# Kernel optimization log

Measured on AMD Instinct MI355X. Metric: run time of the kernel, lower is better.

## Reference

```python
import jax, jax.numpy as jnp
import numpy as np

DIM = 1024
HEADS = 16
HEAD_DIM = DIM // HEADS
B, N, S = 4, 4096, 512


def setup_inputs() -> dict:
    key = jax.random.key(0)
    ks = jax.random.split(key, 9)
    scale = DIM ** -0.5
    return {
        "x": jax.random.normal(ks[0], (B, N, DIM), dtype=jnp.float32),
        "context": jax.random.normal(ks[1], (B, S, DIM), dtype=jnp.float32),
        "context_mask": jax.random.uniform(ks[2], (B, S)) < 0.2,  # True = padding
        "q_w": jax.random.normal(ks[3], (DIM, DIM), dtype=jnp.float32) * scale,
        "q_b": jnp.zeros((DIM,), dtype=jnp.float32),
        "kv_w": jax.random.normal(ks[4], (DIM, 2 * DIM), dtype=jnp.float32) * scale,
        "kv_b": jnp.zeros((2 * DIM,), dtype=jnp.float32),
        "proj_w": jax.random.normal(ks[5], (DIM, DIM), dtype=jnp.float32) * scale,
        "proj_b": jnp.zeros((DIM,), dtype=jnp.float32),
    }


def reference(x, context, context_mask, q_w, q_b, kv_w, kv_b, proj_w, proj_b):
    b, n, c = x.shape
    s = context.shape[1]
    h, d = HEADS, HEAD_DIM
    scale = d ** -0.5

    # projections
    q = (x @ q_w + q_b).reshape(b, n, h, d)            # [B,N,H,D]
    kv = (context @ kv_w + kv_b).reshape(b, s, 2, h, d)
    k = kv[:, :, 0]                                     # [B,S,H,D]
    v = kv[:, :, 1]

    # scores [B,H,N,S]
    attn = jnp.einsum("bnhd,bshd->bhns", q, k) * scale
    attn = jnp.where(context_mask[:, None, None, :], -jnp.inf, attn)
    attn = jax.nn.softmax(attn, axis=-1)

    out = jnp.einsum("bhns,bshd->bnhd", attn, v).reshape(b, n, c)
    return out @ proj_w + proj_b
```

## Files before the change

kernel.cpp:

```cpp
#include <hip/hip_runtime.h>
#include <hip/hip_bf16.h>

typedef __attribute__((ext_vector_type(8))) short bf16x8;
typedef __attribute__((ext_vector_type(4))) float f32x4;
typedef unsigned short u16;

#define DIMC 1024
#define NHEAD 16
#define HDIM 64
#define NB 4
#define NQ 4096
#define NS 512

#define LOG2E 1.44269504f

#if __has_builtin(__builtin_amdgcn_exp2f)
#define EXP2F(x) __builtin_amdgcn_exp2f(x)
#else
#define EXP2F(x) __expf(0.69314718f * (x))
#endif

#if __has_builtin(__builtin_amdgcn_rcpf)
#define RCPF(x) __builtin_amdgcn_rcpf(x)
#else
#define RCPF(x) (1.0f / (x))
#endif

__device__ __forceinline__ u16 f2bf(float f) {
  __hip_bfloat16 h = __float2bfloat16(f);
  return *reinterpret_cast<u16*>(&h);
}

__device__ __forceinline__ unsigned pack_bf2(float a, float b) {
  __hip_bfloat162 h2 = __float22bfloat162_rn(make_float2(a, b));
  return *reinterpret_cast<unsigned*>(&h2);
}

__device__ __forceinline__ void gload_lds16(const void* g, void* s) {
  __builtin_amdgcn_global_load_lds(
      (const __attribute__((address_space(1))) void*)g,
      (__attribute__((address_space(3))) void*)s, 16, 0, 0);
}


__device__ __forceinline__ void cvt_body(const float* __restrict__ in,
                                         u16* __restrict__ out, int base, int nblk,
                                         int n4) {
  const int stride = nblk * 256;
  for (int i = base * 256 + threadIdx.x; i < n4; i += stride) {
    float4 v = *(const float4*)(in + (size_t)i * 4);
    ushort4 o;
    o.x = f2bf(v.x); o.y = f2bf(v.y); o.z = f2bf(v.z); o.w = f2bf(v.w);
    *(ushort4*)(out + (size_t)i * 4) = o;
  }
}

__global__ void prep_kernel(const float* __restrict__ x, const float* __restrict__ ctx,
                            const int* __restrict__ cmask,
                            const float* __restrict__ q_w, const float* __restrict__ kv_w,
                            const float* __restrict__ proj_w,
                            u16* __restrict__ x_bf, u16* __restrict__ ctx_bf,
                            u16* __restrict__ qwT, u16* __restrict__ kvwT,
                            u16* __restrict__ pwT, float* __restrict__ maskf) {
  __shared__ float t[32][33];
  const int bid = blockIdx.x;
  if (bid < 2048) {
    cvt_body(x, x_bf, bid, 2048, 16777216 / 4);
    return;
  }
  if (bid < 2560) {
    cvt_body(ctx, ctx_bf, bid - 2048, 512, 2097152 / 4);
    return;
  }
  if (bid >= 6656) {
    const int i = (bid - 6656) * 256 + threadIdx.x;
    if (i < NB * NS) maskf[i] = cmask[i] ? -1e30f : 0.0f;
    return;
  }
  const float* W;
  u16* WT;
  int K, N, local;
  if (bid < 3584) {
    W = q_w; WT = qwT; K = 1024; N = 1024; local = bid - 2560;
  } else if (bid < 5632) {
    W = kv_w; WT = kvwT; K = 1024; N = 2048; local = bid - 3584;
  } else {
    W = proj_w; WT = pwT; K = 1024; N = 1024; local = bid - 5632;
  }
  const int nbx = N >> 5;
  const int bx = (local % nbx) * 32;
  const int by = (local / nbx) * 32;
  const int tx = threadIdx.x & 31, ty = threadIdx.x >> 5;
#pragma unroll
  for (int i = 0; i < 32; i += 8)
    t[ty + i][tx] = W[(size_t)(by + ty + i) * N + bx + tx];
  __syncthreads();
#pragma unroll
  for (int i = 0; i < 32; i += 8)
    WT[(size_t)(bx + ty + i) * K + by + tx] = f2bf(t[tx][ty + i]);
}


__launch_bounds__(256)
__global__ void gemm_kv(const u16* __restrict__ A, const u16* __restrict__ BT,
                        const float* __restrict__ bias, u16* __restrict__ Kout,
                        u16* __restrict__ VTout, int M, int N, int K) {
  __shared__ __align__(16) u16 As[128 * 32];
  __shared__ __align__(16) u16 Bs[128 * 32];
  const int tid = threadIdx.x;
  const int w = tid >> 6, l = tid & 63;
  const int wr = w >> 1, wc = w & 1;
  const int fr = l & 15, fhi = l >> 4;

  const int nwg = gridDim.x * gridDim.y;
  const int o = blockIdx.y * gridDim.x + blockIdx.x;
  const int tIdx = (o & 7) * (nwg >> 3) + (o >> 3);
  const int m0 = (tIdx / gridDim.x) * 128;
  const int n0 = (tIdx % gridDim.x) * 128;

  const f32x4 fz = {0.f, 0.f, 0.f, 0.f};
  f32x4 acc[4][4];
#pragma unroll
  for (int mt = 0; mt < 4; mt++)
#pragma unroll
    for (int nt = 0; nt < 4; nt++) acc[mt][nt] = fz;

  const int f0 = w * 2048 + l * 16;
  const int f1 = f0 + 1024;
  const int ar0 = f0 >> 6, ac0 = (f0 & 63) >> 1;
  const int ar1 = f1 >> 6, ac1 = (f1 & 63) >> 1;
  const u16* Ag0 = A + (size_t)(m0 + ar0) * K + ac0;
  const u16* Ag1 = A + (size_t)(m0 + ar1) * K + ac1;
  const u16* Bg0 = BT + (size_t)(n0 + ar0) * K + ac0;
  const u16* Bg1 = BT + (size_t)(n0 + ar1) * K + ac1;

  for (int k0 = 0; k0 < K; k0 += 32) {
    gload_lds16(Ag0 + k0, &As[w * 1024]);
    gload_lds16(Ag1 + k0, &As[w * 1024 + 512]);
    gload_lds16(Bg0 + k0, &Bs[w * 1024]);
    gload_lds16(Bg1 + k0, &Bs[w * 1024 + 512]);
    __syncthreads();

    bf16x8 a[4], b[4];
#pragma unroll
    for (int t = 0; t < 4; t++) {
      a[t] = *(const bf16x8*)&As[(wr * 64 + t * 16 + fr) * 32 + fhi * 8];
      b[t] = *(const bf16x8*)&Bs[(wc * 64 + t * 16 + fr) * 32 + fhi * 8];
    }
#pragma unroll
    for (int mt = 0; mt < 4; mt++)
#pragma unroll
      for (int nt = 0; nt < 4; nt++)
        acc[mt][nt] = __builtin_amdgcn_mfma_f32_16x16x32_bf16(a[mt], b[nt], acc[mt][nt], 0, 0, 0);
    __syncthreads();
  }

#pragma unroll
  for (int mt = 0; mt < 4; mt++) {
#pragma unroll
    for (int nt = 0; nt < 4; nt++) {
      const int col = n0 + wc * 64 + nt * 16 + fr;
      const float bv = bias[col];
#pragma unroll
      for (int r = 0; r < 4; r++) {
        const int row = m0 + wr * 64 + mt * 16 + fhi * 4 + r;
        const float v = acc[mt][nt][r] + bv;
        const int b = row >> 9, s = row & 511;
        if (col < 1024) {
          const int h = col >> 6, d = col & 63;
          Kout[(((size_t)(b * 16 + h)) * 512 + s) * 64 + d] = f2bf(v);
        } else {
          const int c2 = col - 1024;
          const int h = c2 >> 6, d = c2 & 63;
          VTout[(((size_t)(b * 16 + h)) * 64 + d) * 512 + s] = f2bf(v);
        }
      }
    }
  }
}


template<int MODE>
__launch_bounds__(512, 1)
__global__ void gemm256(const u16* __restrict__ A, const u16* __restrict__ BT,
                        const float* __restrict__ bias, void* __restrict__ C0,
                        int M, int N, int K) {
  __shared__ __align__(16) u16 As[2][16384];
  __shared__ __align__(16) u16 Bs[2][16384];
  const int tid = threadIdx.x;
  const int w = tid >> 6, l = tid & 63;
  const int wm = w >> 2, wn = w & 3;
  const int fr = l & 15, fhi = l >> 4;

  const int nblk = gridDim.x;
  const int nN = N >> 8;
  const int o = blockIdx.x;
  const int tIdx = (o & 7) * (nblk >> 3) + (o >> 3);
  const int m0 = (tIdx / nN) << 8;
  const int n0 = (tIdx % nN) << 8;

  const int rowoff = tid >> 3;
  const int gchunk = (tid & 7) ^ (rowoff & 7);
  const u16* Abase = A + (size_t)(m0 + rowoff) * K + gchunk * 8;
  const u16* Bbase = BT + (size_t)(n0 + rowoff) * K + gchunk * 8;
  const int ldsoff = w * 512;

  const f32x4 fz = {0.f, 0.f, 0.f, 0.f};
  f32x4 acc[2][4][4];
#pragma unroll
  for (int mh = 0; mh < 2; mh++)
#pragma unroll
    for (int m = 0; m < 4; m++)
#pragma unroll
      for (int n = 0; n < 4; n++) acc[mh][m][n] = fz;

  const int KT = K >> 6;

#pragma unroll
  for (int p = 0; p < 4; ++p) {
    gload_lds16(Abase + (size_t)(p * 64) * K, &As[0][p * 4096 + ldsoff]);
    gload_lds16(Bbase + (size_t)(p * 64) * K, &Bs[0][p * 4096 + ldsoff]);
  }
  asm volatile("s_waitcnt vmcnt(0)" ::: "memory");
  __builtin_amdgcn_s_barrier();

  int nb = 0;
  for (int kt = 0; kt < KT; ++kt) {
    const int knext = (kt + 1) << 6;
    const bool more = (kt + 1) < KT;
#pragma unroll
    for (int p = 0; p < 4; ++p) {
      const int mh = p >> 1, kk = p & 1;
      const int ch = ((kk << 2) | fhi) ^ (fr & 7);
      bf16x8 af[4], bfr[4];
#pragma unroll
      for (int m = 0; m < 4; ++m) {
        const int row = wm * 128 + mh * 64 + m * 16 + fr;
        af[m] = *(const bf16x8*)((const char*)&As[nb][0] + row * 128 + ch * 16);
      }
#pragma unroll
      for (int n = 0; n < 4; ++n) {
        const int row = wn * 64 + n * 16 + fr;
        bfr[n] = *(const bf16x8*)((const char*)&Bs[nb][0] + row * 128 + ch * 16);
      }
      if (more) {
        gload_lds16(Abase + (size_t)(p * 64) * K + knext, &As[nb ^ 1][p * 4096 + ldsoff]);
        gload_lds16(Bbase + (size_t)(p * 64) * K + knext, &Bs[nb ^ 1][p * 4096 + ldsoff]);
      }
      __builtin_amdgcn_s_barrier();
      asm volatile("s_waitcnt lgkmcnt(0)" ::: "memory");
      __builtin_amdgcn_s_setprio(1);
#pragma unroll
      for (int m = 0; m < 4; ++m)
#pragma unroll
        for (int n = 0; n < 4; ++n)
          acc[mh][m][n] = __builtin_amdgcn_mfma_f32_16x16x32_bf16(af[m], bfr[n], acc[mh][m][n], 0, 0, 0);
      __builtin_amdgcn_s_setprio(0);
      __builtin_amdgcn_s_barrier();
    }
    asm volatile("s_waitcnt vmcnt(0)" ::: "memory");
    __builtin_amdgcn_s_barrier();
    nb ^= 1;
  }

#pragma unroll
  for (int mh = 0; mh < 2; ++mh)
#pragma unroll
    for (int m = 0; m < 4; ++m)
#pragma unroll
      for (int n = 0; n < 4; ++n) {
        const int col = n0 + wn * 64 + n * 16 + fr;
        const float bv = bias[col];
#pragma unroll
        for (int r = 0; r < 4; ++r) {
          const int row = m0 + wm * 128 + mh * 64 + m * 16 + fhi * 4 + r;
          const float v = acc[mh][m][n][r] + bv;
          if (MODE == 0)
            ((u16*)C0)[(size_t)row * N + col] = f2bf(v * 0.125f);
          else
            ((float*)C0)[(size_t)row * N + col] = v;
        }
      }
}

__launch_bounds__(512, 2)
__global__ void attn_kernel(const u16* __restrict__ Q, const u16* __restrict__ Kb,
                            const u16* __restrict__ VT, const float* __restrict__ maskf,
                            u16* __restrict__ O) {
  __shared__ __align__(16) u16 Ks[512 * 64];
  __shared__ __align__(16) u16 Vs[64 * 512];
  __shared__ __align__(16) u16 Ps[8][2048];
  const int tid = threadIdx.x, w = tid >> 6, l = tid & 63;
  const int fr = l & 15, fhi = l >> 4;

  const int rid = blockIdx.x;
  const int orig = ((rid & 7) << 5) + (rid >> 3);
  const int bh = orig >> 2, qc = orig & 3;
  const int b = bh >> 4, h = bh & 15;

  const u16* Kg = Kb + (size_t)bh * NS * HDIM;
  const u16* Vg = VT + (size_t)bh * HDIM * NS;
  const float* mrow = maskf + b * NS;

#pragma unroll
  for (int it = 0; it < 8; ++it) {
    const int slot = it * 512 + tid;
    const int r = slot >> 3, c3 = slot & 7;
    const int gc = c3 ^ (r & 7);
    gload_lds16(Kg + (size_t)r * HDIM + gc * 8, &Ks[slot * 8]);
  }
#pragma unroll
  for (int it = 0; it < 8; ++it) {
    const int slot = it * 512 + tid;
    const int r = slot >> 6, c6 = slot & 63;
    const int gc = c6 ^ (r & 7);
    gload_lds16(Vg + (size_t)r * NS + gc * 8, &Vs[slot * 8]);
  }
  asm volatile("s_waitcnt vmcnt(0)" ::: "memory");
  __syncthreads();

  u16* Pw = Ps[w];
  const f32x4 fz = {0.f, 0.f, 0.f, 0.f};

  bf16x8 onesf;
#pragma unroll
  for (int i = 0; i < 8; ++i) onesf[i] = (short)0x3F80;

#pragma unroll 1
  for (int qt2 = 0; qt2 < 2; ++qt2) {
    const int rowbase_a = b * NQ + qc * 1024 + w * 128 + qt2 * 64;
    const int rowbase_b = rowbase_a + 32;

    bf16x8 qfa[2][2], qfb[2][2];
#pragma unroll
    for (int mt = 0; mt < 2; mt++)
#pragma unroll
      for (int kk = 0; kk < 2; kk++) {
        qfa[mt][kk] = *(const bf16x8*)&Q[(size_t)(rowbase_a + mt * 16 + fr) * DIMC +
                                         h * 64 + kk * 32 + fhi * 8];
        qfb[mt][kk] = *(const bf16x8*)&Q[(size_t)(rowbase_b + mt * 16 + fr) * DIMC +
                                         h * 64 + kk * 32 + fhi * 8];
      }

    f32x4 lacc_a[2], lacc_b[2];
    f32x4 oa[2][4], ob[2][4];
#pragma unroll
    for (int mt = 0; mt < 2; mt++) {
      lacc_a[mt] = fz; lacc_b[mt] = fz;
#pragma unroll
      for (int dn = 0; dn < 4; dn++) { oa[mt][dn] = fz; ob[mt][dn] = fz; }
    }

#pragma unroll
    for (int t = 0; t < 8; ++t) {
      const int sc = t * 64;

      bf16x8 kf[2][4];
#pragma unroll
      for (int kk = 0; kk < 2; kk++)
#pragma unroll
        for (int sn = 0; sn < 4; sn++) {
          const int row = sc + sn * 16 + fr;
          const int byte = row * 128 + ((((kk << 2) | fhi) ^ (fr & 7)) << 4);
          kf[kk][sn] = *(const bf16x8*)((const char*)&Ks[0] + byte);
        }

      f32x4 sa[2][4];
#pragma unroll
      for (int mt = 0; mt < 2; mt++)
#pragma unroll
        for (int sn = 0; sn < 4; sn++) sa[mt][sn] = fz;
      __builtin_amdgcn_s_setprio(1);
#pragma unroll
      for (int kk = 0; kk < 2; kk++)
#pragma unroll
        for (int sn = 0; sn < 4; sn++)
#pragma unroll
          for (int mt = 0; mt < 2; mt++)
            sa[mt][sn] = __builtin_amdgcn_mfma_f32_16x16x32_bf16(kf[kk][sn], qfa[mt][kk], sa[mt][sn], 0, 0, 0);
      __builtin_amdgcn_s_setprio(0);

      float4 mv4[4];
#pragma unroll
      for (int sn = 0; sn < 4; sn++)
        mv4[sn] = *(const float4*)&mrow[sc + sn * 16 + fhi * 4];

#pragma unroll
      for (int mt = 0; mt < 2; mt++) {
        const int qrow = mt * 16 + fr;
#pragma unroll
        for (int sn = 0; sn < 4; sn++) {
          const float e0 = EXP2F(fmaf(sa[mt][sn][0], LOG2E, ((const float*)&mv4[sn])[0]));
          const float e1 = EXP2F(fmaf(sa[mt][sn][1], LOG2E, ((const float*)&mv4[sn])[1]));
          const float e2 = EXP2F(fmaf(sa[mt][sn][2], LOG2E, ((const float*)&mv4[sn])[2]));
          const float e3 = EXP2F(fmaf(sa[mt][sn][3], LOG2E, ((const float*)&mv4[sn])[3]));
          int byte = qrow * 128 + sn * 32 + fhi * 8;
          byte ^= (qrow & 7) << 4;
          uint2 pk;
          pk.x = pack_bf2(e0, e1);
          pk.y = pack_bf2(e2, e3);
          *(uint2*)((char*)Pw + byte) = pk;
        }
      }
      asm volatile("s_waitcnt lgkmcnt(0)" ::: "memory");

      bf16x8 vv[2][4];
#pragma unroll
      for (int kk = 0; kk < 2; kk++)
#pragma unroll
        for (int dn = 0; dn < 4; dn++) {
          const int row = dn * 16 + fr;
          const int byte = row * 1024 +
              (((sc >> 3) + ((((kk << 2) | fhi) ^ (fr & 7)))) << 4);
          vv[kk][dn] = *(const bf16x8*)((const char*)&Vs[0] + byte);
        }

      __builtin_amdgcn_s_setprio(1);
#pragma unroll
      for (int kk = 0; kk < 2; kk++)
#pragma unroll
        for (int mt = 0; mt < 2; mt++) {
          int byte = (mt * 16 + fr) * 128 + kk * 64 + fhi * 16;
          byte ^= (fr & 7) << 4;
          const bf16x8 pa = *(const bf16x8*)((char*)Pw + byte);
#pragma unroll
          for (int dn = 0; dn < 4; dn++)
            oa[mt][dn] = __builtin_amdgcn_mfma_f32_16x16x32_bf16(pa, vv[kk][dn], oa[mt][dn], 0, 0, 0);
          lacc_a[mt] = __builtin_amdgcn_mfma_f32_16x16x32_bf16(pa, onesf, lacc_a[mt], 0, 0, 0);
        }
      __builtin_amdgcn_s_setprio(0);

      f32x4 sb[2][4];
#pragma unroll
      for (int mt = 0; mt < 2; mt++)
#pragma unroll
        for (int sn = 0; sn < 4; sn++) sb[mt][sn] = fz;
      __builtin_amdgcn_s_setprio(1);
#pragma unroll
      for (int kk = 0; kk < 2; kk++)
#pragma unroll
        for (int sn = 0; sn < 4; sn++)
#pragma unroll
          for (int mt = 0; mt < 2; mt++)
            sb[mt][sn] = __builtin_amdgcn_mfma_f32_16x16x32_bf16(kf[kk][sn], qfb[mt][kk], sb[mt][sn], 0, 0, 0);
      __builtin_amdgcn_s_setprio(0);

#pragma unroll
      for (int mt = 0; mt < 2; mt++) {
        const int qrow = mt * 16 + fr;
#pragma unroll
        for (int sn = 0; sn < 4; sn++) {
          const float e0 = EXP2F(fmaf(sb[mt][sn][0], LOG2E, ((const float*)&mv4[sn])[0]));
          const float e1 = EXP2F(fmaf(sb[mt][sn][1], LOG2E, ((const float*)&mv4[sn])[1]));
          const float e2 = EXP2F(fmaf(sb[mt][sn][2], LOG2E, ((const float*)&mv4[sn])[2]));
          const float e3 = EXP2F(fmaf(sb[mt][sn][3], LOG2E, ((const float*)&mv4[sn])[3]));
          int byte = qrow * 128 + sn * 32 + fhi * 8;
          byte ^= (qrow & 7) << 4;
          uint2 pk;
          pk.x = pack_bf2(e0, e1);
          pk.y = pack_bf2(e2, e3);
          *(uint2*)((char*)Pw + byte) = pk;
        }
      }
      asm volatile("s_waitcnt lgkmcnt(0)" ::: "memory");

      __builtin_amdgcn_s_setprio(1);
#pragma unroll
      for (int kk = 0; kk < 2; kk++)
#pragma unroll
        for (int mt = 0; mt < 2; mt++) {
          int byte = (mt * 16 + fr) * 128 + kk * 64 + fhi * 16;
          byte ^= (fr & 7) << 4;
          const bf16x8 pa = *(const bf16x8*)((char*)Pw + byte);
#pragma unroll
          for (int dn = 0; dn < 4; dn++)
            ob[mt][dn] = __builtin_amdgcn_mfma_f32_16x16x32_bf16(pa, vv[kk][dn], ob[mt][dn], 0, 0, 0);
          lacc_b[mt] = __builtin_amdgcn_mfma_f32_16x16x32_bf16(pa, onesf, lacc_b[mt], 0, 0, 0);
        }
      __builtin_amdgcn_s_setprio(0);
    }

#pragma unroll
    for (int mt = 0; mt < 2; mt++) {
      float loa[4], lob[4];
#pragma unroll
      for (int r = 0; r < 4; r++) {
        loa[r] = RCPF(lacc_a[mt][r]);
        lob[r] = RCPF(lacc_b[mt][r]);
      }
#pragma unroll
      for (int dn = 0; dn < 4; dn++)
#pragma unroll
        for (int r = 0; r < 4; r++) {
          const int rowa = rowbase_a + mt * 16 + fhi * 4 + r;
          O[(size_t)rowa * DIMC + h * 64 + dn * 16 + fr] = f2bf(oa[mt][dn][r] * loa[r]);
          const int rowb = rowbase_b + mt * 16 + fhi * 4 + r;
          O[(size_t)rowb * DIMC + h * 64 + dn * 16 + fr] = f2bf(ob[mt][dn][r] * lob[r]);
        }
    }
  }
}


extern "C" void kernel_launch(void* const* d_in, const int* in_sizes, int n_in,
                              void* d_out, int out_size, void* d_ws, size_t ws_size,
                              hipStream_t stream) {
  const float* x      = (const float*)d_in[0];
  const float* ctx    = (const float*)d_in[1];
  const int*   cmask  = (const int*)d_in[2];
  const float* q_w    = (const float*)d_in[3];
  const float* q_b    = (const float*)d_in[4];
  const float* kv_w   = (const float*)d_in[5];
  const float* kv_b   = (const float*)d_in[6];
  const float* proj_w = (const float*)d_in[7];
  const float* proj_b = (const float*)d_in[8];
  float* out = (float*)d_out;

  char* ws = (char*)d_ws;
  size_t off = 0;
  auto alloc = [&](size_t bytes) {
    void* p = ws + off;
    off += (bytes + 255) & ~(size_t)255;
    return p;
  };
  u16* x_bf   = (u16*)alloc((size_t)16384 * 1024 * 2);
  u16* ctx_bf = (u16*)alloc((size_t)2048 * 1024 * 2);
  u16* qwT    = (u16*)alloc((size_t)1024 * 1024 * 2);
  u16* kvwT   = (u16*)alloc((size_t)2048 * 1024 * 2);
  u16* pwT    = (u16*)alloc((size_t)1024 * 1024 * 2);
  u16* Qb     = (u16*)alloc((size_t)16384 * 1024 * 2);
  u16* Kbuf   = (u16*)alloc((size_t)64 * 512 * 64 * 2);
  u16* VTbuf  = (u16*)alloc((size_t)64 * 64 * 512 * 2);
  u16* Ob     = (u16*)alloc((size_t)16384 * 1024 * 2);
  float* maskf = (float*)alloc((size_t)NB * NS * 4);

  prep_kernel<<<6664, 256, 0, stream>>>(x, ctx, cmask, q_w, kv_w, proj_w,
                                        x_bf, ctx_bf, qwT, kvwT, pwT, maskf);

  gemm256<0><<<256, 512, 0, stream>>>(x_bf, qwT, q_b, Qb, 16384, 1024, 1024);
  gemm_kv<<<dim3(16, 16), 256, 0, stream>>>(ctx_bf, kvwT, kv_b, Kbuf, VTbuf, 2048, 2048, 1024);
  attn_kernel<<<256, 512, 0, stream>>>(Qb, Kbuf, VTbuf, maskf, Ob);
  gemm256<2><<<256, 512, 0, stream>>>(Ob, pwT, proj_b, out, 16384, 1024, 1024);
}
```

Before: 177.2 us.

## Double-buffer KV projection GEMM with swizzled LDS and drop per-phase barriers

The KV projection GEMM moves from a single-buffered loop with a 32-wide K step to a 64-wide K step. It now double-buffers A and B in LDS, prefetching the next tile while MFMAs run on the current one. Global-to-LDS loads use an XOR chunk swizzle to cut LDS bank conflicts, and MFMAs are wrapped in setprio. Separately, the inner-phase barriers and lgkmcnt wait are removed from the Q/proj GEMM, which relies on the per-tile vmcnt wait and barrier for correctness. That removal risks a race if the prefetch writes into LDS still being read by other waves, and it drops the explicit wait for the LDS fragment reads.

```diff
diff --git a/kernel.cpp b/kernel.cpp
--- a/kernel.cpp
+++ b/kernel.cpp
@@ -105,8 +105,8 @@
 __global__ void gemm_kv(const u16* __restrict__ A, const u16* __restrict__ BT,
                         const float* __restrict__ bias, u16* __restrict__ Kout,
                         u16* __restrict__ VTout, int M, int N, int K) {
-  __shared__ __align__(16) u16 As[128 * 32];
-  __shared__ __align__(16) u16 Bs[128 * 32];
+  __shared__ __align__(16) u16 As[2][8192];
+  __shared__ __align__(16) u16 Bs[2][8192];
   const int tid = threadIdx.x;
   const int w = tid >> 6, l = tid & 63;
   const int wr = w >> 1, wc = w & 1;
@@ -125,34 +125,55 @@
 #pragma unroll
     for (int nt = 0; nt < 4; nt++) acc[mt][nt] = fz;
 
-  const int f0 = w * 2048 + l * 16;
-  const int f1 = f0 + 1024;
-  const int ar0 = f0 >> 6, ac0 = (f0 & 63) >> 1;
-  const int ar1 = f1 >> 6, ac1 = (f1 & 63) >> 1;
-  const u16* Ag0 = A + (size_t)(m0 + ar0) * K + ac0;
-  const u16* Ag1 = A + (size_t)(m0 + ar1) * K + ac1;
-  const u16* Bg0 = BT + (size_t)(n0 + ar0) * K + ac0;
-  const u16* Bg1 = BT + (size_t)(n0 + ar1) * K + ac1;
-
-  for (int k0 = 0; k0 < K; k0 += 32) {
-    gload_lds16(Ag0 + k0, &As[w * 1024]);
-    gload_lds16(Ag1 + k0, &As[w * 1024 + 512]);
-    gload_lds16(Bg0 + k0, &Bs[w * 1024]);
-    gload_lds16(Bg1 + k0, &Bs[w * 1024 + 512]);
-    __syncthreads();
-
-    bf16x8 a[4], b[4];
-#pragma unroll
-    for (int t = 0; t < 4; t++) {
-      a[t] = *(const bf16x8*)&As[(wr * 64 + t * 16 + fr) * 32 + fhi * 8];
-      b[t] = *(const bf16x8*)&Bs[(wc * 64 + t * 16 + fr) * 32 + fhi * 8];
-    }
-#pragma unroll
-    for (int mt = 0; mt < 4; mt++)
-#pragma unroll
-      for (int nt = 0; nt < 4; nt++)
-        acc[mt][nt] = __builtin_amdgcn_mfma_f32_16x16x32_bf16(a[mt], b[nt], acc[mt][nt], 0, 0, 0);
-    __syncthreads();
+  const int rowoff = tid >> 3;
+  const int gchunk = (tid & 7) ^ (rowoff & 7);
+  const u16* Abase = A + (size_t)(m0 + rowoff) * K + gchunk * 8;
+  const u16* Bbase = BT + (size_t)(n0 + rowoff) * K + gchunk * 8;
+  const int ldsoff = w * 512;
+
+  const int KT = K >> 6;
+
+#pragma unroll
+  for (int p = 0; p < 4; ++p) {
+    gload_lds16(Abase + (size_t)(p * 32) * K, &As[0][p * 2048 + ldsoff]);
+    gload_lds16(Bbase + (size_t)(p * 32) * K, &Bs[0][p * 2048 + ldsoff]);
+  }
+  asm volatile("s_waitcnt vmcnt(0)" ::: "memory");
+  __builtin_amdgcn_s_barrier();
+
+  int nb = 0;
+  for (int kt = 0; kt < KT; ++kt) {
+    const int knext = (kt + 1) << 6;
+    const bool more = (kt + 1) < KT;
+    if (more) {
+#pragma unroll
+      for (int p = 0; p < 4; ++p) {
+        gload_lds16(Abase + (size_t)(p * 32) * K + knext, &As[nb ^ 1][p * 2048 + ldsoff]);
+        gload_lds16(Bbase + (size_t)(p * 32) * K + knext, &Bs[nb ^ 1][p * 2048 + ldsoff]);
+      }
+    }
+#pragma unroll
+    for (int kk = 0; kk < 2; ++kk) {
+      const int ch = ((kk << 2) | fhi) ^ (fr & 7);
+      bf16x8 a[4], b[4];
+#pragma unroll
+      for (int t = 0; t < 4; t++) {
+        const int ra = wr * 64 + t * 16 + fr;
+        a[t] = *(const bf16x8*)((const char*)&As[nb][0] + ra * 128 + ch * 16);
+        const int rb = wc * 64 + t * 16 + fr;
+        b[t] = *(const bf16x8*)((const char*)&Bs[nb][0] + rb * 128 + ch * 16);
+      }
+      __builtin_amdgcn_s_setprio(1);
+#pragma unroll
+      for (int mt = 0; mt < 4; mt++)
+#pragma unroll
+        for (int nt = 0; nt < 4; nt++)
+          acc[mt][nt] = __builtin_amdgcn_mfma_f32_16x16x32_bf16(a[mt], b[nt], acc[mt][nt], 0, 0, 0);
+      __builtin_amdgcn_s_setprio(0);
+    }
+    asm volatile("s_waitcnt vmcnt(0)" ::: "memory");
+    __builtin_amdgcn_s_barrier();
+    nb ^= 1;
   }
 
 #pragma unroll
@@ -247,8 +268,6 @@
         gload_lds16(Abase + (size_t)(p * 64) * K + knext, &As[nb ^ 1][p * 4096 + ldsoff]);
         gload_lds16(Bbase + (size_t)(p * 64) * K + knext, &Bs[nb ^ 1][p * 4096 + ldsoff]);
       }
-      __builtin_amdgcn_s_barrier();
-      asm volatile("s_waitcnt lgkmcnt(0)" ::: "memory");
       __builtin_amdgcn_s_setprio(1);
 #pragma unroll
       for (int m = 0; m < 4; ++m)
@@ -256,7 +275,6 @@
         for (int n = 0; n < 4; ++n)
           acc[mh][m][n] = __builtin_amdgcn_mfma_f32_16x16x32_bf16(af[m], bfr[n], acc[mh][m][n], 0, 0, 0);
       __builtin_amdgcn_s_setprio(0);
-      __builtin_amdgcn_s_barrier();
     }
     asm volatile("s_waitcnt vmcnt(0)" ::: "memory");
     __builtin_amdgcn_s_barrier();
```

New measurement: 170.4 us. 1.04x faster.
